# Kernel optimization log

Measured on AMD Instinct MI355X. Metric: run time of the kernel, lower is better.

The kernel has to match this reference:

```python
import jax, jax.numpy as jnp
import numpy as np

B, N, C = 8, 2048, 151  # batch, num rois, n_obj_classes
D_IN = C + 4            # RELPN_WITH_BBOX_INFO adds 4 normalized box coords
HID = 64


def setup_inputs() -> dict:
    key = jax.random.key(0)
    ks = jax.random.split(key, 8)
    # rois: [B, N, 5] = (batch_idx, x1, y1, x2, y2) in pixel coords
    boxes = jax.random.uniform(ks[0], (B, N, 4), dtype=jnp.float32) * 600.0
    rois = jnp.concatenate([jnp.zeros((B, N, 1), jnp.float32), boxes], axis=2)
    roi_feat = jax.random.normal(ks[1], (B, N, C), dtype=jnp.float32)
    im_info = jnp.ones((B, 3), jnp.float32) * 600.0  # (h, w, scale)
    s1 = 1.0 / np.sqrt(D_IN)
    s2 = 1.0 / np.sqrt(HID)
    return {
        "rois": rois,
        "roi_feat": roi_feat,
        "im_info": im_info,
        "w1_sub": jax.random.normal(ks[2], (D_IN, HID), jnp.float32) * s1,
        "b1_sub": jnp.zeros((HID,), jnp.float32),
        "w2_sub": jax.random.normal(ks[3], (HID, HID), jnp.float32) * s2,
        "b2_sub": jnp.zeros((HID,), jnp.float32),
        "w1_obj": jax.random.normal(ks[4], (D_IN, HID), jnp.float32) * s1,
        "b1_obj": jnp.zeros((HID,), jnp.float32),
        "w2_obj": jax.random.normal(ks[5], (HID, HID), jnp.float32) * s2,
        "b2_obj": jnp.zeros((HID,), jnp.float32),
        "K": 2048,
    }


def _mlp(x, w1, b1, w2, b2):
    return jax.nn.relu(x @ w1 + b1) @ w2 + b2


def reference(rois, roi_feat, im_info, w1_sub, b1_sub, w2_sub, b2_sub,
              w1_obj, b1_obj, w2_obj, b2_obj, K):
    b, n, _ = roi_feat.shape
    # normalized bbox info appended to roi features (RELPN_WITH_BBOX_INFO)
    xy = rois[:, :, 1:3] / im_info[:, 1][:, None, None]
    wh = rois[:, :, 3:5] / im_info[:, 0][:, None, None]
    feat = jnp.concatenate([roi_feat, xy, wh], axis=2)  # [B, N, 155]
    feat = jax.lax.stop_gradient(feat)  # original uses roi_feat4prop.detach()
    x_sub = _mlp(feat, w1_sub, b1_sub, w2_sub, b2_sub)  # [B, N, 64]
    x_obj = _mlp(feat, w1_obj, b1_obj, w2_obj, b2_obj)  # [B, N, 64]
    # bilinear pair scores: [B, N, N] -> [B, N*N]
    bil = jnp.einsum("bnd,bmd->bnm", x_sub, x_obj).reshape(b, n * n)
    vis_score = jax.nn.sigmoid(bil)  # [B, N*N]
    # proposal layer: top-K scoring (sub, obj) pairs per image
    top_scores, top_idx = jax.lax.top_k(vis_score, K)  # [B, K]
    sub_idx = top_idx // n
    obj_idx = top_idx % n
    boxes = rois[:, :, 1:5]  # [B, N, 4]
    sub_boxes = jnp.take_along_axis(boxes, sub_idx[:, :, None], axis=1)
    obj_boxes = jnp.take_along_axis(boxes, obj_idx[:, :, None], axis=1)
    roi_pairs = jnp.concatenate([sub_boxes, obj_boxes], axis=2)  # [B, K, 8]
    roi_proposals = jnp.stack([sub_idx, obj_idx], axis=2)        # [B, K, 2]
    return roi_pairs, roi_proposals, top_scores, vis_score
```

## Files before the change

kernel.cpp:

```cpp
#include <hip/hip_runtime.h>
#include <math.h>

#define NB 8
#define NN_ROI 2048
#define C_FEAT 151
#define D_IN 155
#define HID 64
#define K_TOP 2048
#define NN2 (NN_ROI*NN_ROI)
#define CAP 4096
#define NKB 1024
#define SLOTS 131072
#define LCAP 448
#define BM 128
#define BN 128

#define WS_XS    0x0
#define WS_XO    0x400000
#define WS_CNT2  0x800000
#define WS_FLAGS 0x800040
#define WS_CAND2 0x800080
#define WS_NEED  (0x800080 + NB*SLOTS*4)

__global__ __launch_bounds__(256) void mlp_kernel(
    const float* __restrict__ rois, const float* __restrict__ roi_feat,
    const float* __restrict__ im_info,
    const float* __restrict__ w1_sub, const float* __restrict__ b1_sub,
    const float* __restrict__ w2_sub, const float* __restrict__ b2_sub,
    const float* __restrict__ w1_obj, const float* __restrict__ b1_obj,
    const float* __restrict__ w2_obj, const float* __restrict__ b2_obj,
    float* __restrict__ Xs, float* __restrict__ Xo,
    int* __restrict__ cnt2, int* __restrict__ flags)
{
    __shared__ __align__(16) float featL[32][156];
    __shared__ __align__(16) float hL[32][68];
    const int tid   = threadIdx.x;
    const int pass  = blockIdx.x >> 9;
    const int chunk = blockIdx.x & 511;
    const int row0  = chunk * 32;
    const int b     = row0 >> 11;
    const float* w1 = pass ? w1_obj : w1_sub;
    const float* w2 = pass ? w2_obj : w2_sub;
    const float* b1 = pass ? b1_obj : b1_sub;
    const float* b2 = pass ? b2_obj : b2_sub;
    float* X = pass ? Xo : Xs;
    const float im0 = im_info[b*3+0];
    const float im1 = im_info[b*3+1];

    if (blockIdx.x == 0 && tid < 9) {
        if (tid < 8) cnt2[tid] = 0;
        else flags[0] = 0;
    }

    for (int i = tid; i < 32*C_FEAT; i += 256) {
        const int r = i / C_FEAT, d = i - r*C_FEAT;
        featL[r][d] = roi_feat[(size_t)(row0+r)*C_FEAT + d];
    }
    if (tid < 32) {
        const int r = tid;
        #pragma unroll
        for (int c = 0; c < 4; ++c)
            featL[r][C_FEAT+c] = rois[(size_t)(row0+r)*5 + 1 + c] / (c < 2 ? im1 : im0);
    }
    __syncthreads();

    const int tx = tid & 15, ty = tid >> 4;
    float acc[2][4] = {};
    for (int d4 = 0; d4 < 38; ++d4) {
        const int d = d4*4;
        float wv[4][4], fv[2][4];
        #pragma unroll
        for (int q = 0; q < 4; ++q)
            *(float4*)wv[q] = *(const float4*)&w1[(d+q)*HID + tx*4];
        #pragma unroll
        for (int i = 0; i < 2; ++i)
            *(float4*)fv[i] = *(const float4*)&featL[ty*2+i][d];
        #pragma unroll
        for (int q = 0; q < 4; ++q)
            #pragma unroll
            for (int i = 0; i < 2; ++i)
                #pragma unroll
                for (int j = 0; j < 4; ++j)
                    acc[i][j] = fmaf(fv[i][q], wv[q][j], acc[i][j]);
    }
    #pragma unroll
    for (int d = 152; d < 155; ++d) {
        float wv[4];
        *(float4*)wv = *(const float4*)&w1[d*HID + tx*4];
        #pragma unroll
        for (int i = 0; i < 2; ++i) {
            const float f = featL[ty*2+i][d];
            #pragma unroll
            for (int j = 0; j < 4; ++j)
                acc[i][j] = fmaf(f, wv[j], acc[i][j]);
        }
    }
    {
        float b1v[4];
        *(float4*)b1v = *(const float4*)&b1[tx*4];
        #pragma unroll
        for (int i = 0; i < 2; ++i)
            #pragma unroll
            for (int j = 0; j < 4; ++j) {
                const float v = acc[i][j] + b1v[j];
                hL[ty*2+i][tx*4+j] = v > 0.0f ? v : 0.0f;
            }
    }
    __syncthreads();

    float x[2][4] = {};
    for (int k4 = 0; k4 < 16; ++k4) {
        const int k = k4*4;
        float wv[4][4], hv[2][4];
        #pragma unroll
        for (int q = 0; q < 4; ++q)
            *(float4*)wv[q] = *(const float4*)&w2[(k+q)*HID + tx*4];
        #pragma unroll
        for (int i = 0; i < 2; ++i)
            *(float4*)hv[i] = *(const float4*)&hL[ty*2+i][k];
        #pragma unroll
        for (int q = 0; q < 4; ++q)
            #pragma unroll
            for (int i = 0; i < 2; ++i)
                #pragma unroll
                for (int j = 0; j < 4; ++j)
                    x[i][j] = fmaf(hv[i][q], wv[q][j], x[i][j]);
    }
    {
        float b2v[4];
        *(float4*)b2v = *(const float4*)&b2[tx*4];
        #pragma unroll
        for (int i = 0; i < 2; ++i) {
            *(float4*)&X[(size_t)(row0 + ty*2 + i)*HID + tx*4] = make_float4(
                x[i][0]+b2v[0], x[i][1]+b2v[1], x[i][2]+b2v[2], x[i][3]+b2v[3]);
        }
    }
}

__global__ __launch_bounds__(256) void bil_kernel(
    const float* __restrict__ Xs, const float* __restrict__ Xo,
    float* __restrict__ vis, int* __restrict__ cnt2,
    unsigned int* __restrict__ cand2, int* __restrict__ flags)
{
    __shared__ __align__(16) float As[16][128];
    __shared__ __align__(16) float Bs[16][128];
    __shared__ unsigned int lcand[LCAP];
    __shared__ int lcnt, lbase;
    const int tid = threadIdx.x;
    const int tx = tid & 15, ty = tid >> 4;
    const int bm = blockIdx.x * BM, bn = blockIdx.y * BN, b = blockIdx.z;
    if (tid == 0) lcnt = 0;

    const float4* Ag = (const float4*)(Xs + ((size_t)b*NN_ROI + bm)*HID);
    const float4* Bg = (const float4*)(Xo + ((size_t)b*NN_ROI + bn)*HID);

    float acc[8][8];
    #pragma unroll
    for (int i = 0; i < 8; ++i)
        #pragma unroll
        for (int j = 0; j < 8; ++j) acc[i][j] = 0.0f;

    for (int ph = 0; ph < 4; ++ph) {
        if (ph) __syncthreads();
        #pragma unroll
        for (int it = 0; it < 2; ++it) {
            const int lin = it*256 + tid;
            const int r = lin >> 2, k4 = lin & 3;
            const float4 v = Ag[r*16 + ph*4 + k4];
            const int rs = r ^ (k4 << 3);
            As[k4*4+0][rs] = v.x; As[k4*4+1][rs] = v.y;
            As[k4*4+2][rs] = v.z; As[k4*4+3][rs] = v.w;
        }
        #pragma unroll
        for (int it = 0; it < 2; ++it) {
            const int lin = it*256 + tid;
            const int r = lin >> 2, k4 = lin & 3;
            const float4 v = Bg[r*16 + ph*4 + k4];
            const int rs = r ^ (k4 << 3);
            Bs[k4*4+0][rs] = v.x; Bs[k4*4+1][rs] = v.y;
            Bs[k4*4+2][rs] = v.z; Bs[k4*4+3][rs] = v.w;
        }
        __syncthreads();
        #pragma unroll
        for (int k = 0; k < 16; ++k) {
            const int swz = (k >> 2) << 3;
            const int am = (ty*8) ^ swz;
            const float4 a0 = *(const float4*)&As[k][am];
            const float4 a1 = *(const float4*)&As[k][am + 4];
            const float4 q0 = *(const float4*)&Bs[k][(tx*4) ^ swz];
            const float4 q1 = *(const float4*)&Bs[k][(64 + tx*4) ^ swz];
            const float a[8]  = {a0.x,a0.y,a0.z,a0.w,a1.x,a1.y,a1.z,a1.w};
            const float bb[8] = {q0.x,q0.y,q0.z,q0.w,q1.x,q1.y,q1.z,q1.w};
            #pragma unroll
            for (int i = 0; i < 8; ++i)
                #pragma unroll
                for (int j = 0; j < 8; ++j)
                    acc[i][j] = fmaf(a[i], bb[j], acc[i][j]);
        }
    }

    const size_t visbase = (size_t)b * NN2;
    #pragma unroll
    for (int i = 0; i < 8; ++i) {
        const int row = bm + ty*8 + i;
        float f[8];
        #pragma unroll
        for (int j = 0; j < 8; ++j) {
            const float xv = acc[i][j];
            const float e = __expf(-xv);
            f[j] = __builtin_amdgcn_rcpf(1.0f + e);
            if (xv >= 9.0f) {
                const float se = 1.0f / (1.0f + e);
                const int ku = 0x3F800000 - __float_as_int(se);
                if (ku < NKB) {
                    const int col = bn + (j < 4 ? tx*4 + j : 64 + tx*4 + (j-4));
                    const unsigned int key =
                        ((unsigned int)ku << 22) | (unsigned int)(row*NN_ROI + col);
                    const int p = atomicAdd(&lcnt, 1);
                    if (p < LCAP) lcand[p] = key;
                    else {
                        const int gp = atomicAdd(&cnt2[b], 1);
                        if (gp < SLOTS) cand2[(size_t)b*SLOTS + gp] = key;
                    }
                }
            }
        }
        *(float4*)&vis[visbase + (size_t)row*NN_ROI + bn + tx*4] =
            make_float4(f[0], f[1], f[2], f[3]);
        *(float4*)&vis[visbase + (size_t)row*NN_ROI + bn + 64 + tx*4] =
            make_float4(f[4], f[5], f[6], f[7]);
    }
    __syncthreads();
    int n = lcnt; if (n > LCAP) n = LCAP;
    if (tid == 0) lbase = atomicAdd(&cnt2[b], n);
    __syncthreads();
    const int bs = lbase;
    for (int i = tid; i < n; i += 256) {
        const int p = bs + i;
        if (p < SLOTS) cand2[(size_t)b*SLOTS + p] = lcand[i];
    }
}

__global__ __launch_bounds__(1024) void topk_kernel(
    const int* __restrict__ cnt2, const unsigned int* __restrict__ cand2,
    const float* __restrict__ rois,
    float* __restrict__ pairs, float* __restrict__ props, float* __restrict__ scores,
    int* __restrict__ flags)
{
    __shared__ unsigned int key[CAP];
    __shared__ int hist[NKB];
    __shared__ int part[64];
    __shared__ int scnt;
    __shared__ int kTsh;
    const int b = blockIdx.x, tid = threadIdx.x;
    int M = cnt2[b]; if (M > SLOTS) M = SLOTS;
    if (cnt2[b] > SLOTS) atomicOr(flags, 4);

    for (int i = tid; i < NKB; i += 1024) hist[i] = 0;
    if (tid == 0) scnt = 0;
    __syncthreads();
    for (int i = tid; i < M; i += 1024)
        atomicAdd(&hist[cand2[(size_t)b*SLOTS + i] >> 22], 1);
    __syncthreads();
    if (tid < 64) {
        int s = 0;
        for (int i = 0; i < 16; ++i) s += hist[tid*16 + i];
        part[tid] = s;
    }
    __syncthreads();
    if (tid == 0) {
        int cum = 0, kT = NKB - 1; bool found = false;
        for (int c = 0; c < 64; ++c) {
            if (cum + part[c] >= K_TOP) {
                for (int i = c*16; i < c*16 + 16; ++i) {
                    cum += hist[i];
                    if (cum >= K_TOP) { kT = i; found = true; break; }
                }
                break;
            }
            cum += part[c];
        }
        if (!found) atomicOr(flags, 16);
        kTsh = kT;
    }
    __syncthreads();
    const unsigned long long kl = ((unsigned long long)(kTsh + 1)) << 22;
    for (int c = tid; c < CAP; c += 1024) key[c] = 0xFFFFFFFFu;
    __syncthreads();
    for (int i = tid; i < M; i += 1024) {
        const unsigned int k = cand2[(size_t)b*SLOTS + i];
        if ((unsigned long long)k < kl) {
            const int p = atomicAdd(&scnt, 1);
            if (p < CAP) key[p] = k;
        }
    }
    __syncthreads();
    if (tid == 0) {
        if (scnt < K_TOP) atomicOr(flags, 2);
        if (scnt > CAP)   atomicOr(flags, 4);
    }
    for (int kk = 2; kk <= CAP; kk <<= 1)
        for (int j = kk >> 1; j > 0; j >>= 1) {
            for (int t = tid; t < CAP/2; t += 1024) {
                const int i = 2*t - (t & (j-1));
                const int p = i + j;
                const bool up = (i & kk) == 0;
                const unsigned int a = key[i], c2 = key[p];
                if (up ? (a > c2) : (a < c2)) { key[i] = c2; key[p] = a; }
            }
            __syncthreads();
        }
    for (int k = tid; k < K_TOP-1; k += 1024)
        if (key[k] >= key[k+1]) atomicOr(flags, 8);
    for (int k = tid; k < K_TOP; k += 1024) {
        const unsigned int kw = key[k];
        const int idx = (int)(kw & 0x3FFFFFu);
        const int ku  = (int)(kw >> 22);
        const int sub = idx >> 11, obj = idx & (NN_ROI-1);
        const float sc = __int_as_float(0x3F800000 - ku);
        const float* rs = rois + ((size_t)b*NN_ROI + sub)*5 + 1;
        const float* ro = rois + ((size_t)b*NN_ROI + obj)*5 + 1;
        const size_t o = (size_t)b*K_TOP + k;
        *(float4*)&pairs[o*8]   = make_float4(rs[0],rs[1],rs[2],rs[3]);
        *(float4*)&pairs[o*8+4] = make_float4(ro[0],ro[1],ro[2],ro[3]);
        props[o*2]   = (float)sub;
        props[o*2+1] = (float)obj;
        scores[o]    = sc;
    }
    __syncthreads();
    if (tid == 0) {
        const int f = atomicOr(flags, 0);
        if (f) pairs[0] = 1e5f * (float)f;
    }
}

__global__ void sentinel_kernel(float* out) { out[0] = 1e5f; }

extern "C" void kernel_launch(void* const* d_in, const int* in_sizes, int n_in,
                              void* d_out, int out_size, void* d_ws, size_t ws_size,
                              hipStream_t stream)
{
    static const int EXP_SIZES[12] = {81920, 2473984, 24, 9920, 64, 4096, 64,
                                      9920, 64, 4096, 64, 1};
    bool ok = (n_in == 12) && (out_size == 33734656) && (ws_size >= (size_t)WS_NEED);
    if (ok) for (int i = 0; i < 12; ++i) if (in_sizes[i] != EXP_SIZES[i]) { ok = false; break; }
    if (!ok) { sentinel_kernel<<<1, 1, 0, stream>>>((float*)d_out); return; }

    const float* rois     = (const float*)d_in[0];
    const float* roi_feat = (const float*)d_in[1];
    const float* im_info  = (const float*)d_in[2];
    const float* w1_sub   = (const float*)d_in[3];
    const float* b1_sub   = (const float*)d_in[4];
    const float* w2_sub   = (const float*)d_in[5];
    const float* b2_sub   = (const float*)d_in[6];
    const float* w1_obj   = (const float*)d_in[7];
    const float* b1_obj   = (const float*)d_in[8];
    const float* w2_obj   = (const float*)d_in[9];
    const float* b2_obj   = (const float*)d_in[10];

    char* ws = (char*)d_ws;
    float* Xs           = (float*)(ws + WS_XS);
    float* Xo           = (float*)(ws + WS_XO);
    int* cnt2           = (int*)  (ws + WS_CNT2);
    int* flags          = (int*)  (ws + WS_FLAGS);
    unsigned int* cand2 = (unsigned int*)(ws + WS_CAND2);

    float* out    = (float*)d_out;
    float* pairs  = out;
    float* props  = out + 131072;
    float* scores = out + 163840;
    float* vis    = out + 180224;

    mlp_kernel<<<1024, 256, 0, stream>>>(rois, roi_feat, im_info,
        w1_sub, b1_sub, w2_sub, b2_sub, w1_obj, b1_obj, w2_obj, b2_obj,
        Xs, Xo, cnt2, flags);
    bil_kernel<<<dim3(16, 16, NB), 256, 0, stream>>>(Xs, Xo, vis, cnt2, cand2, flags);
    topk_kernel<<<NB, 1024, 0, stream>>>(cnt2, cand2, rois, pairs, props, scores, flags);
}
```

Measured before the change: 156.6 us.

## Store Xs transposed and read A operand via wave-uniform scalar loads in bilinear GEMM

```diff
diff --git a/kernel.cpp b/kernel.cpp
--- a/kernel.cpp
+++ b/kernel.cpp
@@ -8,6 +8,7 @@
 #define HID 64
 #define K_TOP 2048
 #define NN2 (NN_ROI*NN_ROI)
+#define NROWS (NB*NN_ROI)
 #define CAP 4096
 #define NKB 1024
 #define SLOTS 131072
@@ -15,7 +16,7 @@
 #define BM 128
 #define BN 128
 
-#define WS_XS    0x0
+#define WS_XST   0x0
 #define WS_XO    0x400000
 #define WS_CNT2  0x800000
 #define WS_FLAGS 0x800040
@@ -29,7 +30,7 @@
     const float* __restrict__ w2_sub, const float* __restrict__ b2_sub,
     const float* __restrict__ w1_obj, const float* __restrict__ b1_obj,
     const float* __restrict__ w2_obj, const float* __restrict__ b2_obj,
-    float* __restrict__ Xs, float* __restrict__ Xo,
+    float* __restrict__ XsT, float* __restrict__ Xo,
     int* __restrict__ cnt2, int* __restrict__ flags)
 {
     __shared__ __align__(16) float featL[32][156];
@@ -43,7 +44,6 @@
     const float* w2 = pass ? w2_obj : w2_sub;
     const float* b1 = pass ? b1_obj : b1_sub;
     const float* b2 = pass ? b2_obj : b2_sub;
-    float* X = pass ? Xo : Xs;
     const float im0 = im_info[b*3+0];
     const float im1 = im_info[b*3+1];
 
@@ -129,93 +129,84 @@
     {
         float b2v[4];
         *(float4*)b2v = *(const float4*)&b2[tx*4];
-        #pragma unroll
-        for (int i = 0; i < 2; ++i) {
-            *(float4*)&X[(size_t)(row0 + ty*2 + i)*HID + tx*4] = make_float4(
-                x[i][0]+b2v[0], x[i][1]+b2v[1], x[i][2]+b2v[2], x[i][3]+b2v[3]);
+        if (pass == 0) {
+            #pragma unroll
+            for (int i = 0; i < 2; ++i)
+                #pragma unroll
+                for (int j = 0; j < 4; ++j)
+                    XsT[(size_t)(tx*4+j)*NROWS + row0 + ty*2 + i] = x[i][j] + b2v[j];
+        } else {
+            #pragma unroll
+            for (int i = 0; i < 2; ++i)
+                *(float4*)&Xo[(size_t)(row0 + ty*2 + i)*HID + tx*4] = make_float4(
+                    x[i][0]+b2v[0], x[i][1]+b2v[1], x[i][2]+b2v[2], x[i][3]+b2v[3]);
         }
     }
 }
 
 __global__ __launch_bounds__(256) void bil_kernel(
-    const float* __restrict__ Xs, const float* __restrict__ Xo,
+    const float* __restrict__ XsT, const float* __restrict__ Xo,
     float* __restrict__ vis, int* __restrict__ cnt2,
     unsigned int* __restrict__ cand2, int* __restrict__ flags)
 {
-    __shared__ __align__(16) float As[16][128];
-    __shared__ __align__(16) float Bs[16][128];
+    __shared__ __align__(16) float Bs[64][128];
     __shared__ unsigned int lcand[LCAP];
     __shared__ int lcnt, lbase;
-    const int tid = threadIdx.x;
-    const int tx = tid & 15, ty = tid >> 4;
+    const int tid  = threadIdx.x;
+    const int lane = tid & 63;
+    const int w    = __builtin_amdgcn_readfirstlane(tid >> 6);
     const int bm = blockIdx.x * BM, bn = blockIdx.y * BN, b = blockIdx.z;
     if (tid == 0) lcnt = 0;
 
-    const float4* Ag = (const float4*)(Xs + ((size_t)b*NN_ROI + bm)*HID);
     const float4* Bg = (const float4*)(Xo + ((size_t)b*NN_ROI + bn)*HID);
-
-    float acc[8][8];
     #pragma unroll
-    for (int i = 0; i < 8; ++i)
-        #pragma unroll
-        for (int j = 0; j < 8; ++j) acc[i][j] = 0.0f;
-
-    for (int ph = 0; ph < 4; ++ph) {
-        if (ph) __syncthreads();
-        #pragma unroll
-        for (int it = 0; it < 2; ++it) {
-            const int lin = it*256 + tid;
-            const int r = lin >> 2, k4 = lin & 3;
-            const float4 v = Ag[r*16 + ph*4 + k4];
-            const int rs = r ^ (k4 << 3);
-            As[k4*4+0][rs] = v.x; As[k4*4+1][rs] = v.y;
-            As[k4*4+2][rs] = v.z; As[k4*4+3][rs] = v.w;
-        }
-        #pragma unroll
-        for (int it = 0; it < 2; ++it) {
-            const int lin = it*256 + tid;
-            const int r = lin >> 2, k4 = lin & 3;
-            const float4 v = Bg[r*16 + ph*4 + k4];
-            const int rs = r ^ (k4 << 3);
-            Bs[k4*4+0][rs] = v.x; Bs[k4*4+1][rs] = v.y;
-            Bs[k4*4+2][rs] = v.z; Bs[k4*4+3][rs] = v.w;
-        }
-        __syncthreads();
-        #pragma unroll
-        for (int k = 0; k < 16; ++k) {
-            const int swz = (k >> 2) << 3;
-            const int am = (ty*8) ^ swz;
-            const float4 a0 = *(const float4*)&As[k][am];
-            const float4 a1 = *(const float4*)&As[k][am + 4];
-            const float4 q0 = *(const float4*)&Bs[k][(tx*4) ^ swz];
-            const float4 q1 = *(const float4*)&Bs[k][(64 + tx*4) ^ swz];
-            const float a[8]  = {a0.x,a0.y,a0.z,a0.w,a1.x,a1.y,a1.z,a1.w};
-            const float bb[8] = {q0.x,q0.y,q0.z,q0.w,q1.x,q1.y,q1.z,q1.w};
-            #pragma unroll
-            for (int i = 0; i < 8; ++i)
-                #pragma unroll
-                for (int j = 0; j < 8; ++j)
-                    acc[i][j] = fmaf(a[i], bb[j], acc[i][j]);
+    for (int it = 0; it < 8; ++it) {
+        const int lin = it*256 + tid;
+        const int r = lin >> 4, k4 = lin & 15;
+        const float4 v = Bg[r*16 + k4];
+        const int rs = r ^ ((k4 & 7) << 2);
+        Bs[k4*4+0][rs] = v.x; Bs[k4*4+1][rs] = v.y;
+        Bs[k4*4+2][rs] = v.z; Bs[k4*4+3][rs] = v.w;
+    }
+    __syncthreads();
+
+    const float* At = XsT + (size_t)b*NN_ROI + bm + 32*w;
+
+    float acc[32][2];
+    #pragma unroll
+    for (int r = 0; r < 32; ++r) { acc[r][0] = 0.0f; acc[r][1] = 0.0f; }
+
+    #pragma unroll 2
+    for (int k = 0; k < 64; ++k) {
+        const float* ak = At + (size_t)k*NROWS;
+        const int ci = (2*lane) ^ (((k >> 2) & 7) << 2);
+        const float2 bv = *(const float2*)&Bs[k][ci];
+        #pragma unroll
+        for (int r = 0; r < 32; ++r) {
+            const float av = ak[r];
+            acc[r][0] = fmaf(av, bv.x, acc[r][0]);
+            acc[r][1] = fmaf(av, bv.y, acc[r][1]);
         }
     }
 
     const size_t visbase = (size_t)b * NN2;
-    #pragma unroll
-    for (int i = 0; i < 8; ++i) {
-        const int row = bm + ty*8 + i;
-        float f[8];
-        #pragma unroll
-        for (int j = 0; j < 8; ++j) {
-            const float xv = acc[i][j];
+    const int col0 = bn + 2*lane;
+    #pragma unroll 4
+    for (int r = 0; r < 32; ++r) {
+        const int row = bm + 32*w + r;
+        float f[2];
+        #pragma unroll
+        for (int c = 0; c < 2; ++c) {
+            const float xv = acc[r][c];
             const float e = __expf(-xv);
-            f[j] = __builtin_amdgcn_rcpf(1.0f + e);
+            f[c] = __builtin_amdgcn_rcpf(1.0f + e);
             if (xv >= 9.0f) {
                 const float se = 1.0f / (1.0f + e);
                 const int ku = 0x3F800000 - __float_as_int(se);
                 if (ku < NKB) {
-                    const int col = bn + (j < 4 ? tx*4 + j : 64 + tx*4 + (j-4));
                     const unsigned int key =
-                        ((unsigned int)ku << 22) | (unsigned int)(row*NN_ROI + col);
+                        ((unsigned int)ku << 22) |
+                        (unsigned int)(row*NN_ROI + col0 + c);
                     const int p = atomicAdd(&lcnt, 1);
                     if (p < LCAP) lcand[p] = key;
                     else {
@@ -225,10 +216,7 @@
                 }
             }
         }
-        *(float4*)&vis[visbase + (size_t)row*NN_ROI + bn + tx*4] =
-            make_float4(f[0], f[1], f[2], f[3]);
-        *(float4*)&vis[visbase + (size_t)row*NN_ROI + bn + 64 + tx*4] =
-            make_float4(f[4], f[5], f[6], f[7]);
+        *(float2*)&vis[visbase + (size_t)row*NN_ROI + col0] = make_float2(f[0], f[1]);
     }
     __syncthreads();
     int n = lcnt; if (n > LCAP) n = LCAP;
@@ -359,7 +347,7 @@
     const float* b2_obj   = (const float*)d_in[10];
 
     char* ws = (char*)d_ws;
-    float* Xs           = (float*)(ws + WS_XS);
+    float* XsT          = (float*)(ws + WS_XST);
     float* Xo           = (float*)(ws + WS_XO);
     int* cnt2           = (int*)  (ws + WS_CNT2);
     int* flags          = (int*)  (ws + WS_FLAGS);
@@ -373,7 +361,7 @@
 
     mlp_kernel<<<1024, 256, 0, stream>>>(rois, roi_feat, im_info,
         w1_sub, b1_sub, w2_sub, b2_sub, w1_obj, b1_obj, w2_obj, b2_obj,
-        Xs, Xo, cnt2, flags);
-    bil_kernel<<<dim3(16, 16, NB), 256, 0, stream>>>(Xs, Xo, vis, cnt2, cand2, flags);
+        XsT, Xo, cnt2, flags);
+    bil_kernel<<<dim3(16, 16, NB), 256, 0, stream>>>(XsT, Xo, vis, cnt2, cand2, flags);
     topk_kernel<<<NB, 1024, 0, stream>>>(cnt2, cand2, rois, pairs, props, scores, flags);
 }
```

New measurement: 198.6 us. +26.8%, slower.
